# Optimization experiments

Hardware: AMD Instinct MI355X
Metric: run time of the kernel (lower is better)

## Reference

```python
import jax, jax.numpy as jnp
import numpy as np

V, C, E, L, M = 100000, 420000, 1260000, 3, 64
FV = FC = 3
ED = 2


def _gru(x, h, wih, whh, bih, bhh):
    # PyTorch GRUCell semantics. x: [N, in], h: [N, H], wih: [3H, in], whh: [3H, H]
    gi = x @ wih.T + bih
    gh = h @ whh.T + bhh
    H = h.shape[-1]
    r = jax.nn.sigmoid(gi[:, :H] + gh[:, :H])
    z = jax.nn.sigmoid(gi[:, H:2 * H] + gh[:, H:2 * H])
    n = jnp.tanh(gi[:, 2 * H:] + r * gh[:, 2 * H:])
    return (1.0 - z) * n + z * h


def setup_inputs() -> dict:
    key = jax.random.key(0)
    ks = iter(jax.random.split(key, 40))
    f = lambda shape, s=0.1: jax.random.normal(next(ks), shape, jnp.float32) * s
    inp = {
        'var_features': jax.random.normal(next(ks), (V, FV), jnp.float32),
        'clause_features': jax.random.normal(next(ks), (C, FC), jnp.float32),
        'edge_features': jax.random.uniform(next(ks), (E, ED), dtype=jnp.float32),
        'v2c_w1': f((L, M, FV + ED)), 'v2c_b1': f((L, M)),
        'v2c_w2': f((L, M, M)), 'v2c_b2': f((L, M)),
        'c2v_w1': f((L, M, FC + ED)), 'c2v_b1': f((L, M)),
        'c2v_w2': f((L, M, M)), 'c2v_b2': f((L, M)),
        'var_gru_wih': f((L, 3 * FV, M)), 'var_gru_whh': f((L, 3 * FV, FV)),
        'var_gru_bih': f((L, 3 * FV)), 'var_gru_bhh': f((L, 3 * FV)),
        'cls_gru_wih': f((L, 3 * FC, M)), 'cls_gru_whh': f((L, 3 * FC, FC)),
        'cls_gru_bih': f((L, 3 * FC)), 'cls_gru_bhh': f((L, 3 * FC)),
        'att_w1': f((L, M, FC)), 'att_b1': f((L, M)),
        'att_w2': f((L, 1, M)), 'att_b2': f((L, 1)),
        'var_idx': jax.random.randint(next(ks), (E,), 0, V),
        'clause_idx': jax.random.randint(next(ks), (E,), 0, C),
    }
    return inp


def reference(var_features, clause_features, edge_features,
              v2c_w1, v2c_b1, v2c_w2, v2c_b2,
              c2v_w1, c2v_b1, c2v_w2, c2v_b2,
              var_gru_wih, var_gru_whh, var_gru_bih, var_gru_bhh,
              cls_gru_wih, cls_gru_whh, cls_gru_bih, cls_gru_bhh,
              att_w1, att_b1, att_w2, att_b2,
              var_idx, clause_idx):
    vf, cf = var_features, clause_features
    for l in range(L):  # fixed small number of message-passing steps
        # var -> clause: gather, edge MLP, attention-weight, scatter-add
        v2c_in = jnp.concatenate([vf[var_idx], edge_features], axis=1)  # [E, FV+ED]
        m = jnp.maximum(v2c_in @ v2c_w1[l].T + v2c_b1[l], 0.0) @ v2c_w2[l].T + v2c_b2[l]  # [E, M]
        att = (jnp.tanh(cf @ att_w1[l].T + att_b1[l]) @ att_w2[l].T + att_b2[l])[:, 0]  # [C]
        att = jax.nn.softmax(att, axis=0)
        m = m * att[clause_idx][:, None]
        cmsg = jax.ops.segment_sum(m, clause_idx, num_segments=C)  # [C, M]
        cf_new = _gru(cmsg, cf, cls_gru_wih[l], cls_gru_whh[l], cls_gru_bih[l], cls_gru_bhh[l])
        # clause -> var uses OLD clause features (matches torch forward ordering)
        c2v_in = jnp.concatenate([cf[clause_idx], edge_features], axis=1)  # [E, FC+ED]
        mv = jnp.maximum(c2v_in @ c2v_w1[l].T + c2v_b1[l], 0.0) @ c2v_w2[l].T + c2v_b2[l]  # [E, M]
        vmsg = jax.ops.segment_sum(mv, var_idx, num_segments=V)  # [V, M]
        vf = _gru(vmsg, vf, var_gru_wih[l], var_gru_whh[l], var_gru_bih[l], var_gru_bhh[l])
        cf = cf_new
    return jnp.concatenate([vf, cf], axis=0)  # [V+C, 3]
```

## Files before the change

### kernel.cpp

```cpp
#include <hip/hip_runtime.h>
#include <hip/hip_fp16.h>
#include <math.h>

#define V_N 100000
#define C_N 420000
#define E_N 1260000
#define L_N 3

__device__ __forceinline__ float fsig(float x) {
    return 1.0f / (1.0f + __expf(-x));
}
__device__ __forceinline__ float ftanh(float x) {
    x = fminf(fmaxf(x, -15.0f), 15.0f);
    float t = __expf(2.0f * x);
    return (t - 1.0f) / (t + 1.0f);
}

__global__ void k_prep(const float* __restrict__ v2c_w1, const float* __restrict__ v2c_b1,
                       const float* __restrict__ v2c_w2, const float* __restrict__ v2c_b2,
                       const float* __restrict__ c2v_w1, const float* __restrict__ c2v_b1,
                       const float* __restrict__ c2v_w2, const float* __restrict__ c2v_b2,
                       const float* __restrict__ cls_wih, const float* __restrict__ var_wih,
                       float* __restrict__ prep) {
    int t = blockIdx.x * blockDim.x + threadIdx.x;
    if (t >= 6 * 1040) return;
    int s = t / 1040, r = t % 1040;
    int side = s / 3, l = s % 3;
    const float* w1  = (side ? c2v_w1 : v2c_w1) + l * 320;
    const float* b1  = (side ? c2v_b1 : v2c_b1) + l * 64;
    const float* W2  = (side ? c2v_w2 : v2c_w2) + l * 4096;
    const float* b2  = (side ? c2v_b2 : v2c_b2) + l * 64;
    const float* wih = (side ? var_wih : cls_wih) + l * 576;
    float v = 0.0f;
    if (r < 1024) {
        int j = r >> 4, q = r & 15;
        if (q < 5) v = w1[j * 5 + q];
        else if (q == 5) v = b1[j];
        else if (q < 15) {
            int k = q - 6; float a = 0.0f;
            for (int o = 0; o < 64; ++o) a += wih[k * 64 + o] * W2[o * 64 + j];
            v = a;
        }
    } else if (r < 1033) {
        int k = r - 1024; float a = 0.0f;
        for (int o = 0; o < 64; ++o) a += wih[k * 64 + o] * b2[o];
        v = a;
    }
    prep[t] = v;
}

__global__ __launch_bounds__(256) void k_countrank(const int* __restrict__ ci,
                                                   const int* __restrict__ vi,
                                                   int* __restrict__ cntC, int* __restrict__ cntV,
                                                   int* __restrict__ rankC, int* __restrict__ rankV) {
    int e = blockIdx.x * 256 + threadIdx.x;
    if (e >= E_N) return;
    rankC[e] = atomicAdd(&cntC[ci[e]], 1);
    rankV[e] = atomicAdd(&cntV[vi[e]], 1);
}

__global__ __launch_bounds__(256) void k_scanA(const int* __restrict__ cntC,
                                               const int* __restrict__ cntV, int nbC,
                                               int* __restrict__ bsumC, int* __restrict__ bsumV) {
    int b = blockIdx.x, t = threadIdx.x;
    const int* cnt; int N; int* bs; int bb;
    if (b < nbC) { cnt = cntC; N = C_N; bs = bsumC; bb = b; }
    else         { cnt = cntV; N = V_N; bs = bsumV; bb = b - nbC; }
    int base = bb * 1024 + t * 4;
    int s = 0;
    #pragma unroll
    for (int q = 0; q < 4; ++q) { int i = base + q; if (i < N) s += cnt[i]; }
    __shared__ int sh[256];
    sh[t] = s; __syncthreads();
    for (int d = 128; d; d >>= 1) { if (t < d) sh[t] += sh[t + d]; __syncthreads(); }
    if (t == 0) bs[bb] = sh[0];
}

__global__ __launch_bounds__(512) void k_scanB(int* __restrict__ bsumC, int nbC, int* __restrict__ totC,
                                               int* __restrict__ bsumV, int nbV, int* __restrict__ totV) {
    int* bsum = blockIdx.x ? bsumV : bsumC;
    int nb    = blockIdx.x ? nbV : nbC;
    int* tot  = blockIdx.x ? totV : totC;
    __shared__ int sh[512];
    int t = threadIdx.x;
    int v = (t < nb) ? bsum[t] : 0;
    sh[t] = v; __syncthreads();
    for (int d = 1; d < 512; d <<= 1) {
        int add = (t >= d) ? sh[t - d] : 0;
        __syncthreads();
        sh[t] += add;
        __syncthreads();
    }
    if (t < nb) bsum[t] = sh[t] - v;
    if (t == nb - 1) *tot = sh[t];
}

__global__ __launch_bounds__(256) void k_scanC(const int* __restrict__ cntC,
                                               const int* __restrict__ cntV, int nbC,
                                               const int* __restrict__ bsumC,
                                               const int* __restrict__ bsumV,
                                               int* __restrict__ rowC, int* __restrict__ rowV) {
    int b = blockIdx.x, t = threadIdx.x;
    const int* cnt; int N; const int* bs; int* row; int bb;
    if (b < nbC) { cnt = cntC; N = C_N; bs = bsumC; row = rowC; bb = b; }
    else         { cnt = cntV; N = V_N; bs = bsumV; row = rowV; bb = b - nbC; }
    int base = bb * 1024 + t * 4;
    int v[4], local[4];
    #pragma unroll
    for (int q = 0; q < 4; ++q) { int i = base + q; v[q] = (i < N) ? cnt[i] : 0; }
    local[0] = 0; local[1] = v[0]; local[2] = v[0] + v[1]; local[3] = v[0] + v[1] + v[2];
    int mysum = local[3] + v[3];
    __shared__ int sh[256];
    sh[t] = mysum; __syncthreads();
    for (int d = 1; d < 256; d <<= 1) {
        int add = (t >= d) ? sh[t - d] : 0;
        __syncthreads();
        sh[t] += add;
        __syncthreads();
    }
    int excl = sh[t] - mysum + bs[bb];
    #pragma unroll
    for (int q = 0; q < 4; ++q) {
        int i = base + q;
        if (i < N) row[i] = excl + local[q];
    }
}

__global__ __launch_bounds__(256) void k_att(const float* __restrict__ cf,
                                             const float* __restrict__ aw1,
                                             const float* __restrict__ ab1,
                                             const float* __restrict__ aw2,
                                             const float* __restrict__ ab2,
                                             float* __restrict__ logits,
                                             float* __restrict__ pmax,
                                             float* __restrict__ Sg) {
    if (blockIdx.x == 0 && threadIdx.x == 0) Sg[0] = 0.0f;
    int c = blockIdx.x * blockDim.x + threadIdx.x;
    float logit = -1e30f;
    if (c < C_N) {
        float h0 = cf[c * 3], h1 = cf[c * 3 + 1], h2 = cf[c * 3 + 2];
        float acc = ab2[0];
        #pragma unroll
        for (int k = 0; k < 64; ++k) {
            float tv = ftanh(aw1[k * 3] * h0 + aw1[k * 3 + 1] * h1 +
                             aw1[k * 3 + 2] * h2 + ab1[k]);
            acc += aw2[k] * tv;
        }
        logits[c] = acc;
        logit = acc;
    }
    float m = logit;
    #pragma unroll
    for (int off = 32; off; off >>= 1) m = fmaxf(m, __shfl_xor(m, off));
    __shared__ float smax[4];
    int lane = threadIdx.x & 63, wid = threadIdx.x >> 6;
    if (lane == 0) smax[wid] = m;
    __syncthreads();
    if (threadIdx.x == 0)
        pmax[blockIdx.x] = fmaxf(fmaxf(smax[0], smax[1]), fmaxf(smax[2], smax[3]));
}

__global__ __launch_bounds__(256) void k_sum(const float* __restrict__ logits,
                                             const float* __restrict__ pmax, int npmax,
                                             float* __restrict__ Sg) {
    __shared__ float sh[4];
    float m = -1e30f;
    for (int i = threadIdx.x; i < npmax; i += 256) m = fmaxf(m, pmax[i]);
    #pragma unroll
    for (int off = 32; off; off >>= 1) m = fmaxf(m, __shfl_xor(m, off));
    int lane = threadIdx.x & 63, wid = threadIdx.x >> 6;
    if (lane == 0) sh[wid] = m;
    __syncthreads();
    float mm = fmaxf(fmaxf(sh[0], sh[1]), fmaxf(sh[2], sh[3]));
    __syncthreads();
    int c = blockIdx.x * 256 + threadIdx.x;
    float e = (c < C_N) ? __expf(logits[c] - mm) : 0.0f;
    #pragma unroll
    for (int off = 32; off; off >>= 1) e += __shfl_xor(e, off);
    if (lane == 0) sh[wid] = e;
    __syncthreads();
    if (threadIdx.x == 0) {
        unsafeAtomicAdd(&Sg[0], sh[0] + sh[1] + sh[2] + sh[3]);
        if (blockIdx.x == 0) Sg[1] = mm;
    }
}

__global__ __launch_bounds__(256) void k_edge(const float* __restrict__ feat,
                                              const float* __restrict__ ef,
                                              const int* __restrict__ gidx,
                                              const int* __restrict__ didx,
                                              const int* __restrict__ row,
                                              const int* __restrict__ rank,
                                              const float* __restrict__ prep,
                                              uint2* __restrict__ umsg) {
    __shared__ float W[1040];
    for (int i = threadIdx.x; i < 1040; i += 256) W[i] = prep[i];
    __syncthreads();
    int e = blockIdx.x * 256 + threadIdx.x;
    if (e >= E_N) return;
    int g = gidx[e];
    int pos = row[didx[e]] + rank[e];
    float x0 = feat[g * 3], x1 = feat[g * 3 + 1], x2 = feat[g * 3 + 2];
    float2 efv = *(const float2*)(ef + 2 * (size_t)e);
    float u[9];
    #pragma unroll
    for (int k = 0; k < 9; ++k) u[k] = 0.0f;
    for (int j = 0; j < 64; ++j) {
        const float* wj = &W[j * 16];
        float h = wj[0] * x0 + wj[1] * x1 + wj[2] * x2 + wj[3] * efv.x + wj[4] * efv.y + wj[5];
        h = fmaxf(h, 0.0f);
        #pragma unroll
        for (int k = 0; k < 9; ++k) u[k] += wj[6 + k] * h;
    }
    union { __half h[12]; uint2 q[3]; } pk;
    #pragma unroll
    for (int k = 0; k < 9; ++k) pk.h[k] = __float2half(u[k]);
    pk.h[9] = pk.h[10] = pk.h[11] = __float2half(0.0f);
    size_t p = (size_t)pos * 3;
    umsg[p] = pk.q[0]; umsg[p + 1] = pk.q[1]; umsg[p + 2] = pk.q[2];
}

template <bool ATT>
__global__ __launch_bounds__(256) void k_node(const uint2* __restrict__ umsg,
                                              const int* __restrict__ row,
                                              const float* __restrict__ hin,
                                              const float* __restrict__ logits,
                                              const float* __restrict__ Sg,
                                              const float* __restrict__ c2,
                                              const float* __restrict__ whh,
                                              const float* __restrict__ bih,
                                              const float* __restrict__ bhh,
                                              float* __restrict__ hout, int N) {
    int i = blockIdx.x * 256 + threadIdx.x;
    if (i >= N) return;
    int p0 = row[i], p1 = row[i + 1];
    float u[9];
    #pragma unroll
    for (int k = 0; k < 9; ++k) u[k] = 0.0f;
    for (int p = p0; p < p1; ++p) {
        union { __half h[12]; uint2 q[3]; } pk;
        const uint2* r = umsg + (size_t)p * 3;
        pk.q[0] = r[0]; pk.q[1] = r[1]; pk.q[2] = r[2];
        #pragma unroll
        for (int k = 0; k < 9; ++k) u[k] += __half2float(pk.h[k]);
    }
    float cnt = (float)(p1 - p0);
    float scale = 1.0f;
    if (ATT) scale = __expf(logits[i] - Sg[1]) / Sg[0];
    float h0 = hin[i * 3], h1 = hin[i * 3 + 1], h2 = hin[i * 3 + 2];
    float gi[9], gh[9];
    #pragma unroll
    for (int k = 0; k < 9; ++k) gi[k] = scale * (u[k] + cnt * c2[k]) + bih[k];
    #pragma unroll
    for (int k = 0; k < 9; ++k)
        gh[k] = whh[k * 3] * h0 + whh[k * 3 + 1] * h1 + whh[k * 3 + 2] * h2 + bhh[k];
    float r0 = fsig(gi[0] + gh[0]), r1 = fsig(gi[1] + gh[1]), r2 = fsig(gi[2] + gh[2]);
    float z0 = fsig(gi[3] + gh[3]), z1 = fsig(gi[4] + gh[4]), z2 = fsig(gi[5] + gh[5]);
    float n0 = ftanh(gi[6] + r0 * gh[6]);
    float n1 = ftanh(gi[7] + r1 * gh[7]);
    float n2 = ftanh(gi[8] + r2 * gh[8]);
    hout[i * 3 + 0] = (1.0f - z0) * n0 + z0 * h0;
    hout[i * 3 + 1] = (1.0f - z1) * n1 + z1 * h1;
    hout[i * 3 + 2] = (1.0f - z2) * n2 + z2 * h2;
}

extern "C" void kernel_launch(void* const* d_in, const int* in_sizes, int n_in,
                              void* d_out, int out_size, void* d_ws, size_t ws_size,
                              hipStream_t stream) {
    const float* vf0     = (const float*)d_in[0];
    const float* cf0     = (const float*)d_in[1];
    const float* ef      = (const float*)d_in[2];
    const float* v2c_w1  = (const float*)d_in[3];
    const float* v2c_b1  = (const float*)d_in[4];
    const float* v2c_w2  = (const float*)d_in[5];
    const float* v2c_b2  = (const float*)d_in[6];
    const float* c2v_w1  = (const float*)d_in[7];
    const float* c2v_b1  = (const float*)d_in[8];
    const float* c2v_w2  = (const float*)d_in[9];
    const float* c2v_b2  = (const float*)d_in[10];
    const float* var_wih = (const float*)d_in[11];
    const float* var_whh = (const float*)d_in[12];
    const float* var_bih = (const float*)d_in[13];
    const float* var_bhh = (const float*)d_in[14];
    const float* cls_wih = (const float*)d_in[15];
    const float* cls_whh = (const float*)d_in[16];
    const float* cls_bih = (const float*)d_in[17];
    const float* cls_bhh = (const float*)d_in[18];
    const float* att_w1  = (const float*)d_in[19];
    const float* att_b1  = (const float*)d_in[20];
    const float* att_w2  = (const float*)d_in[21];
    const float* att_b2  = (const float*)d_in[22];
    const int*   var_idx = (const int*)d_in[23];
    const int*   cls_idx = (const int*)d_in[24];
    float* dout = (float*)d_out;

    char* w = (char*)d_ws;
    auto alloc = [&](size_t bytes) { char* p = w; w += (bytes + 255) & ~(size_t)255; return p; };
    int*   rowC   = (int*)alloc((C_N + 1) * 4);
    int*   rowV   = (int*)alloc((V_N + 1) * 4);
    int*   cntC   = (int*)alloc((size_t)C_N * 4);
    int*   cntV   = (int*)alloc((size_t)V_N * 4);
    char*  cntEnd = w;
    int*   rankC  = (int*)alloc((size_t)E_N * 4);
    int*   rankV  = (int*)alloc((size_t)E_N * 4);
    int*   bsumC  = (int*)alloc(512 * 4);
    int*   bsumV  = (int*)alloc(512 * 4);
    float* logits = (float*)alloc((size_t)C_N * 4);
    float* pmax   = (float*)alloc(2048 * 4);
    float* Sg     = (float*)alloc(64 * 4);
    float* prep   = (float*)alloc(6 * 1040 * 4);
    uint2* umsg   = (uint2*)alloc((size_t)E_N * 3 * 8);
    float* vfA    = (float*)alloc((size_t)V_N * 3 * 4);
    float* vfB    = (float*)alloc((size_t)V_N * 3 * 4);
    float* cfA    = (float*)alloc((size_t)C_N * 3 * 4);
    float* cfB    = (float*)alloc((size_t)C_N * 3 * 4);

    const int nE  = (E_N + 255) / 256;
    const int nC  = (C_N + 255) / 256;
    const int nV  = (V_N + 255) / 256;
    const int nbC = (C_N + 1023) / 1024;
    const int nbV = (V_N + 1023) / 1024;

    k_prep<<<(6 * 1040 + 255) / 256, 256, 0, stream>>>(
        v2c_w1, v2c_b1, v2c_w2, v2c_b2, c2v_w1, c2v_b1, c2v_w2, c2v_b2,
        cls_wih, var_wih, prep);

    hipMemsetAsync(cntC, 0, (size_t)(cntEnd - (char*)cntC), stream);
    k_countrank<<<nE, 256, 0, stream>>>(cls_idx, var_idx, cntC, cntV, rankC, rankV);
    k_scanA<<<nbC + nbV, 256, 0, stream>>>(cntC, cntV, nbC, bsumC, bsumV);
    k_scanB<<<2, 512, 0, stream>>>(bsumC, nbC, rowC + C_N, bsumV, nbV, rowV + V_N);
    k_scanC<<<nbC + nbV, 256, 0, stream>>>(cntC, cntV, nbC, bsumC, bsumV, rowC, rowV);

    const float* vf_cur = vf0;
    const float* cf_cur = cf0;
    for (int l = 0; l < L_N; ++l) {
        float* vf_next = (l == 0) ? vfA : (l == 1) ? vfB : dout;
        float* cf_next = (l == 0) ? cfA : (l == 1) ? cfB : (dout + (size_t)V_N * 3);

        k_att<<<nC, 256, 0, stream>>>(cf_cur, att_w1 + l * 192, att_b1 + l * 64,
                                      att_w2 + l * 64, att_b2 + l, logits, pmax, Sg);
        k_sum<<<nC, 256, 0, stream>>>(logits, pmax, nC, Sg);

        k_edge<<<nE, 256, 0, stream>>>(vf_cur, ef, var_idx, cls_idx, rowC, rankC,
                                       prep + (0 * 3 + l) * 1040, umsg);
        k_node<true><<<nC, 256, 0, stream>>>(umsg, rowC, cf_cur, logits, Sg,
                                             prep + (0 * 3 + l) * 1040 + 1024,
                                             cls_whh + l * 27, cls_bih + l * 9,
                                             cls_bhh + l * 9, cf_next, C_N);

        k_edge<<<nE, 256, 0, stream>>>(cf_cur, ef, cls_idx, var_idx, rowV, rankV,
                                       prep + (1 * 3 + l) * 1040, umsg);
        k_node<false><<<nV, 256, 0, stream>>>(umsg, rowV, vf_cur, logits, Sg,
                                              prep + (1 * 3 + l) * 1040 + 1024,
                                              var_whh + l * 27, var_bih + l * 9,
                                              var_bhh + l * 9, vf_next, V_N);

        vf_cur = vf_next;
        cf_cur = cf_next;
    }
}
```

Measured before the change: 926.7 us.

## Fuse both edge directions, the softmax sum and next-layer attention into two kernels per layer

```diff
diff --git a/kernel.cpp b/kernel.cpp
--- a/kernel.cpp
+++ b/kernel.cpp
@@ -6,6 +6,9 @@
 #define C_N 420000
 #define E_N 1260000
 #define L_N 3
+#define NCBLK 1641
+#define NVBLK 391
+#define NEBLK 4922
 
 __device__ __forceinline__ float fsig(float x) {
     return 1.0f / (1.0f + __expf(-x));
@@ -126,15 +129,15 @@
     }
 }
 
-__global__ __launch_bounds__(256) void k_att(const float* __restrict__ cf,
-                                             const float* __restrict__ aw1,
-                                             const float* __restrict__ ab1,
-                                             const float* __restrict__ aw2,
-                                             const float* __restrict__ ab2,
-                                             float* __restrict__ logits,
-                                             float* __restrict__ pmax,
-                                             float* __restrict__ Sg) {
-    if (blockIdx.x == 0 && threadIdx.x == 0) Sg[0] = 0.0f;
+__global__ __launch_bounds__(256) void k_att0(const float* __restrict__ cf,
+                                              const float* __restrict__ aw1,
+                                              const float* __restrict__ ab1,
+                                              const float* __restrict__ aw2,
+                                              const float* __restrict__ ab2,
+                                              float* __restrict__ logits,
+                                              float* __restrict__ pmax,
+                                              float* __restrict__ Sg) {
+    if (blockIdx.x == 0 && threadIdx.x < 8) Sg[threadIdx.x] = 0.0f;
     int c = blockIdx.x * blockDim.x + threadIdx.x;
     float logit = -1e30f;
     if (c < C_N) {
@@ -160,108 +163,193 @@
         pmax[blockIdx.x] = fmaxf(fmaxf(smax[0], smax[1]), fmaxf(smax[2], smax[3]));
 }
 
-__global__ __launch_bounds__(256) void k_sum(const float* __restrict__ logits,
-                                             const float* __restrict__ pmax, int npmax,
-                                             float* __restrict__ Sg) {
-    __shared__ float sh[4];
-    float m = -1e30f;
-    for (int i = threadIdx.x; i < npmax; i += 256) m = fmaxf(m, pmax[i]);
-    #pragma unroll
-    for (int off = 32; off; off >>= 1) m = fmaxf(m, __shfl_xor(m, off));
-    int lane = threadIdx.x & 63, wid = threadIdx.x >> 6;
-    if (lane == 0) sh[wid] = m;
-    __syncthreads();
-    float mm = fmaxf(fmaxf(sh[0], sh[1]), fmaxf(sh[2], sh[3]));
-    __syncthreads();
-    int c = blockIdx.x * 256 + threadIdx.x;
-    float e = (c < C_N) ? __expf(logits[c] - mm) : 0.0f;
-    #pragma unroll
-    for (int off = 32; off; off >>= 1) e += __shfl_xor(e, off);
-    if (lane == 0) sh[wid] = e;
-    __syncthreads();
-    if (threadIdx.x == 0) {
-        unsafeAtomicAdd(&Sg[0], sh[0] + sh[1] + sh[2] + sh[3]);
-        if (blockIdx.x == 0) Sg[1] = mm;
-    }
-}
-
-__global__ __launch_bounds__(256) void k_edge(const float* __restrict__ feat,
-                                              const float* __restrict__ ef,
-                                              const int* __restrict__ gidx,
-                                              const int* __restrict__ didx,
-                                              const int* __restrict__ row,
-                                              const int* __restrict__ rank,
-                                              const float* __restrict__ prep,
-                                              uint2* __restrict__ umsg) {
-    __shared__ float W[1040];
-    for (int i = threadIdx.x; i < 1040; i += 256) W[i] = prep[i];
+__global__ __launch_bounds__(256) void k_edgeM(const float* __restrict__ vf,
+                                               const float* __restrict__ cf,
+                                               const float* __restrict__ ef,
+                                               const int* __restrict__ var_idx,
+                                               const int* __restrict__ cls_idx,
+                                               const int* __restrict__ rowC,
+                                               const int* __restrict__ rowV,
+                                               const int* __restrict__ rankC,
+                                               const int* __restrict__ rankV,
+                                               const float* __restrict__ prepA,
+                                               const float* __restrict__ prepB,
+                                               const float* __restrict__ logits,
+                                               const float* __restrict__ pmax,
+                                               float* __restrict__ SgL,
+                                               uint2* __restrict__ umsgC,
+                                               uint2* __restrict__ umsgV) {
+    __shared__ float WA[1040], WB[1040];
+    for (int i = threadIdx.x; i < 1040; i += 256) { WA[i] = prepA[i]; WB[i] = prepB[i]; }
     __syncthreads();
     int e = blockIdx.x * 256 + threadIdx.x;
-    if (e >= E_N) return;
-    int g = gidx[e];
-    int pos = row[didx[e]] + rank[e];
-    float x0 = feat[g * 3], x1 = feat[g * 3 + 1], x2 = feat[g * 3 + 2];
-    float2 efv = *(const float2*)(ef + 2 * (size_t)e);
-    float u[9];
-    #pragma unroll
-    for (int k = 0; k < 9; ++k) u[k] = 0.0f;
-    for (int j = 0; j < 64; ++j) {
-        const float* wj = &W[j * 16];
-        float h = wj[0] * x0 + wj[1] * x1 + wj[2] * x2 + wj[3] * efv.x + wj[4] * efv.y + wj[5];
-        h = fmaxf(h, 0.0f);
-        #pragma unroll
-        for (int k = 0; k < 9; ++k) u[k] += wj[6 + k] * h;
-    }
-    union { __half h[12]; uint2 q[3]; } pk;
-    #pragma unroll
-    for (int k = 0; k < 9; ++k) pk.h[k] = __float2half(u[k]);
-    pk.h[9] = pk.h[10] = pk.h[11] = __float2half(0.0f);
-    size_t p = (size_t)pos * 3;
-    umsg[p] = pk.q[0]; umsg[p + 1] = pk.q[1]; umsg[p + 2] = pk.q[2];
-}
-
-template <bool ATT>
-__global__ __launch_bounds__(256) void k_node(const uint2* __restrict__ umsg,
-                                              const int* __restrict__ row,
-                                              const float* __restrict__ hin,
-                                              const float* __restrict__ logits,
-                                              const float* __restrict__ Sg,
-                                              const float* __restrict__ c2,
-                                              const float* __restrict__ whh,
-                                              const float* __restrict__ bih,
-                                              const float* __restrict__ bhh,
-                                              float* __restrict__ hout, int N) {
-    int i = blockIdx.x * 256 + threadIdx.x;
-    if (i >= N) return;
-    int p0 = row[i], p1 = row[i + 1];
-    float u[9];
-    #pragma unroll
-    for (int k = 0; k < 9; ++k) u[k] = 0.0f;
-    for (int p = p0; p < p1; ++p) {
+    if (e < E_N) {
+        int v = var_idx[e], c = cls_idx[e];
+        float2 efv = *(const float2*)(ef + 2 * (size_t)e);
+        float a0 = vf[v * 3], a1 = vf[v * 3 + 1], a2 = vf[v * 3 + 2];
+        float b0 = cf[c * 3], b1 = cf[c * 3 + 1], b2 = cf[c * 3 + 2];
+        float uC[9], uV[9];
+        #pragma unroll
+        for (int k = 0; k < 9; ++k) { uC[k] = 0.0f; uV[k] = 0.0f; }
+        for (int j = 0; j < 64; ++j) {
+            const float* wj = &WA[j * 16];
+            float h = fmaxf(wj[0] * a0 + wj[1] * a1 + wj[2] * a2 +
+                            wj[3] * efv.x + wj[4] * efv.y + wj[5], 0.0f);
+            const float* qj = &WB[j * 16];
+            float g = fmaxf(qj[0] * b0 + qj[1] * b1 + qj[2] * b2 +
+                            qj[3] * efv.x + qj[4] * efv.y + qj[5], 0.0f);
+            #pragma unroll
+            for (int k = 0; k < 9; ++k) { uC[k] += wj[6 + k] * h; uV[k] += qj[6 + k] * g; }
+        }
         union { __half h[12]; uint2 q[3]; } pk;
-        const uint2* r = umsg + (size_t)p * 3;
-        pk.q[0] = r[0]; pk.q[1] = r[1]; pk.q[2] = r[2];
-        #pragma unroll
-        for (int k = 0; k < 9; ++k) u[k] += __half2float(pk.h[k]);
-    }
-    float cnt = (float)(p1 - p0);
-    float scale = 1.0f;
-    if (ATT) scale = __expf(logits[i] - Sg[1]) / Sg[0];
-    float h0 = hin[i * 3], h1 = hin[i * 3 + 1], h2 = hin[i * 3 + 2];
-    float gi[9], gh[9];
-    #pragma unroll
-    for (int k = 0; k < 9; ++k) gi[k] = scale * (u[k] + cnt * c2[k]) + bih[k];
-    #pragma unroll
-    for (int k = 0; k < 9; ++k)
-        gh[k] = whh[k * 3] * h0 + whh[k * 3 + 1] * h1 + whh[k * 3 + 2] * h2 + bhh[k];
-    float r0 = fsig(gi[0] + gh[0]), r1 = fsig(gi[1] + gh[1]), r2 = fsig(gi[2] + gh[2]);
-    float z0 = fsig(gi[3] + gh[3]), z1 = fsig(gi[4] + gh[4]), z2 = fsig(gi[5] + gh[5]);
-    float n0 = ftanh(gi[6] + r0 * gh[6]);
-    float n1 = ftanh(gi[7] + r1 * gh[7]);
-    float n2 = ftanh(gi[8] + r2 * gh[8]);
-    hout[i * 3 + 0] = (1.0f - z0) * n0 + z0 * h0;
-    hout[i * 3 + 1] = (1.0f - z1) * n1 + z1 * h1;
-    hout[i * 3 + 2] = (1.0f - z2) * n2 + z2 * h2;
+        #pragma unroll
+        for (int k = 0; k < 9; ++k) pk.h[k] = __float2half(uC[k]);
+        pk.h[9] = pk.h[10] = pk.h[11] = __float2half(0.0f);
+        size_t pC = (size_t)(rowC[c] + rankC[e]) * 3;
+        umsgC[pC] = pk.q[0]; umsgC[pC + 1] = pk.q[1]; umsgC[pC + 2] = pk.q[2];
+        #pragma unroll
+        for (int k = 0; k < 9; ++k) pk.h[k] = __float2half(uV[k]);
+        size_t pV = (size_t)(rowV[v] + rankV[e]) * 3;
+        umsgV[pV] = pk.q[0]; umsgV[pV + 1] = pk.q[1]; umsgV[pV + 2] = pk.q[2];
+    }
+    if (blockIdx.x < NCBLK) {
+        __shared__ float sh[4];
+        float m = -1e30f;
+        for (int i = threadIdx.x; i < NCBLK; i += 256) m = fmaxf(m, pmax[i]);
+        #pragma unroll
+        for (int off = 32; off; off >>= 1) m = fmaxf(m, __shfl_xor(m, off));
+        int lane = threadIdx.x & 63, wid = threadIdx.x >> 6;
+        if (lane == 0) sh[wid] = m;
+        __syncthreads();
+        float mm = fmaxf(fmaxf(sh[0], sh[1]), fmaxf(sh[2], sh[3]));
+        __syncthreads();
+        int c = blockIdx.x * 256 + threadIdx.x;
+        float ex = (c < C_N) ? __expf(logits[c] - mm) : 0.0f;
+        #pragma unroll
+        for (int off = 32; off; off >>= 1) ex += __shfl_xor(ex, off);
+        if (lane == 0) sh[wid] = ex;
+        __syncthreads();
+        if (threadIdx.x == 0) {
+            unsafeAtomicAdd(&SgL[0], sh[0] + sh[1] + sh[2] + sh[3]);
+            if (blockIdx.x == 0) SgL[1] = mm;
+        }
+    }
+}
+
+__global__ __launch_bounds__(256) void k_nodeM(const uint2* __restrict__ umsgC,
+                                               const uint2* __restrict__ umsgV,
+                                               const int* __restrict__ rowC,
+                                               const int* __restrict__ rowV,
+                                               const float* __restrict__ cfin,
+                                               const float* __restrict__ vfin,
+                                               float* __restrict__ cfout,
+                                               float* __restrict__ vfout,
+                                               const float* __restrict__ SgL,
+                                               float* __restrict__ logits,
+                                               float* __restrict__ pmax,
+                                               const float* __restrict__ c2C,
+                                               const float* __restrict__ c2V,
+                                               const float* __restrict__ cls_whh,
+                                               const float* __restrict__ cls_bih,
+                                               const float* __restrict__ cls_bhh,
+                                               const float* __restrict__ var_whh,
+                                               const float* __restrict__ var_bih,
+                                               const float* __restrict__ var_bhh,
+                                               const float* __restrict__ aw1,
+                                               const float* __restrict__ ab1,
+                                               const float* __restrict__ aw2,
+                                               const float* __restrict__ ab2,
+                                               int do_att) {
+    int b = blockIdx.x;
+    if (b < NCBLK) {
+        int i = b * 256 + threadIdx.x;
+        float logit = -1e30f;
+        if (i < C_N) {
+            int p0 = rowC[i], p1 = rowC[i + 1];
+            float u[9];
+            #pragma unroll
+            for (int k = 0; k < 9; ++k) u[k] = 0.0f;
+            for (int p = p0; p < p1; ++p) {
+                union { __half h[12]; uint2 q[3]; } pk;
+                const uint2* r = umsgC + (size_t)p * 3;
+                pk.q[0] = r[0]; pk.q[1] = r[1]; pk.q[2] = r[2];
+                #pragma unroll
+                for (int k = 0; k < 9; ++k) u[k] += __half2float(pk.h[k]);
+            }
+            float cnt = (float)(p1 - p0);
+            float scale = __expf(logits[i] - SgL[1]) / SgL[0];
+            float h0 = cfin[i * 3], h1 = cfin[i * 3 + 1], h2 = cfin[i * 3 + 2];
+            float gi[9], gh[9];
+            #pragma unroll
+            for (int k = 0; k < 9; ++k) gi[k] = scale * (u[k] + cnt * c2C[k]) + cls_bih[k];
+            #pragma unroll
+            for (int k = 0; k < 9; ++k)
+                gh[k] = cls_whh[k * 3] * h0 + cls_whh[k * 3 + 1] * h1 + cls_whh[k * 3 + 2] * h2 + cls_bhh[k];
+            float r0 = fsig(gi[0] + gh[0]), r1 = fsig(gi[1] + gh[1]), r2 = fsig(gi[2] + gh[2]);
+            float z0 = fsig(gi[3] + gh[3]), z1 = fsig(gi[4] + gh[4]), z2 = fsig(gi[5] + gh[5]);
+            float n0 = ftanh(gi[6] + r0 * gh[6]);
+            float n1 = ftanh(gi[7] + r1 * gh[7]);
+            float n2 = ftanh(gi[8] + r2 * gh[8]);
+            float o0 = (1.0f - z0) * n0 + z0 * h0;
+            float o1 = (1.0f - z1) * n1 + z1 * h1;
+            float o2 = (1.0f - z2) * n2 + z2 * h2;
+            cfout[i * 3 + 0] = o0;
+            cfout[i * 3 + 1] = o1;
+            cfout[i * 3 + 2] = o2;
+            if (do_att) {
+                float acc = ab2[0];
+                #pragma unroll
+                for (int k = 0; k < 64; ++k) {
+                    float tv = ftanh(aw1[k * 3] * o0 + aw1[k * 3 + 1] * o1 +
+                                     aw1[k * 3 + 2] * o2 + ab1[k]);
+                    acc += aw2[k] * tv;
+                }
+                logits[i] = acc;
+                logit = acc;
+            }
+        }
+        if (do_att) {
+            float m = logit;
+            #pragma unroll
+            for (int off = 32; off; off >>= 1) m = fmaxf(m, __shfl_xor(m, off));
+            __shared__ float smax[4];
+            int lane = threadIdx.x & 63, wid = threadIdx.x >> 6;
+            if (lane == 0) smax[wid] = m;
+            __syncthreads();
+            if (threadIdx.x == 0)
+                pmax[b] = fmaxf(fmaxf(smax[0], smax[1]), fmaxf(smax[2], smax[3]));
+        }
+    } else {
+        int i = (b - NCBLK) * 256 + threadIdx.x;
+        if (i >= V_N) return;
+        int p0 = rowV[i], p1 = rowV[i + 1];
+        float u[9];
+        #pragma unroll
+        for (int k = 0; k < 9; ++k) u[k] = 0.0f;
+        for (int p = p0; p < p1; ++p) {
+            union { __half h[12]; uint2 q[3]; } pk;
+            const uint2* r = umsgV + (size_t)p * 3;
+            pk.q[0] = r[0]; pk.q[1] = r[1]; pk.q[2] = r[2];
+            #pragma unroll
+            for (int k = 0; k < 9; ++k) u[k] += __half2float(pk.h[k]);
+        }
+        float cnt = (float)(p1 - p0);
+        float h0 = vfin[i * 3], h1 = vfin[i * 3 + 1], h2 = vfin[i * 3 + 2];
+        float gi[9], gh[9];
+        #pragma unroll
+        for (int k = 0; k < 9; ++k) gi[k] = u[k] + cnt * c2V[k] + var_bih[k];
+        #pragma unroll
+        for (int k = 0; k < 9; ++k)
+            gh[k] = var_whh[k * 3] * h0 + var_whh[k * 3 + 1] * h1 + var_whh[k * 3 + 2] * h2 + var_bhh[k];
+        float r0 = fsig(gi[0] + gh[0]), r1 = fsig(gi[1] + gh[1]), r2 = fsig(gi[2] + gh[2]);
+        float z0 = fsig(gi[3] + gh[3]), z1 = fsig(gi[4] + gh[4]), z2 = fsig(gi[5] + gh[5]);
+        float n0 = ftanh(gi[6] + r0 * gh[6]);
+        float n1 = ftanh(gi[7] + r1 * gh[7]);
+        float n2 = ftanh(gi[8] + r2 * gh[8]);
+        vfout[i * 3 + 0] = (1.0f - z0) * n0 + z0 * h0;
+        vfout[i * 3 + 1] = (1.0f - z1) * n1 + z1 * h1;
+        vfout[i * 3 + 2] = (1.0f - z2) * n2 + z2 * h2;
+    }
 }
 
 extern "C" void kernel_launch(void* const* d_in, const int* in_sizes, int n_in,
@@ -309,15 +397,11 @@
     float* pmax   = (float*)alloc(2048 * 4);
     float* Sg     = (float*)alloc(64 * 4);
     float* prep   = (float*)alloc(6 * 1040 * 4);
-    uint2* umsg   = (uint2*)alloc((size_t)E_N * 3 * 8);
-    float* vfA    = (float*)alloc((size_t)V_N * 3 * 4);
-    float* vfB    = (float*)alloc((size_t)V_N * 3 * 4);
-    float* cfA    = (float*)alloc((size_t)C_N * 3 * 4);
-    float* cfB    = (float*)alloc((size_t)C_N * 3 * 4);
-
-    const int nE  = (E_N + 255) / 256;
-    const int nC  = (C_N + 255) / 256;
-    const int nV  = (V_N + 255) / 256;
+    uint2* umsgC  = (uint2*)alloc((size_t)E_N * 3 * 8);
+    uint2* umsgV  = (uint2*)alloc((size_t)E_N * 3 * 8);
+    float* vfW    = (float*)alloc((size_t)V_N * 3 * 4);
+    float* cfW    = (float*)alloc((size_t)C_N * 3 * 4);
+
     const int nbC = (C_N + 1023) / 1024;
     const int nbV = (V_N + 1023) / 1024;
 
@@ -326,36 +410,36 @@
         cls_wih, var_wih, prep);
 
     hipMemsetAsync(cntC, 0, (size_t)(cntEnd - (char*)cntC), stream);
-    k_countrank<<<nE, 256, 0, stream>>>(cls_idx, var_idx, cntC, cntV, rankC, rankV);
+    k_countrank<<<NEBLK, 256, 0, stream>>>(cls_idx, var_idx, cntC, cntV, rankC, rankV);
     k_scanA<<<nbC + nbV, 256, 0, stream>>>(cntC, cntV, nbC, bsumC, bsumV);
     k_scanB<<<2, 512, 0, stream>>>(bsumC, nbC, rowC + C_N, bsumV, nbV, rowV + V_N);
     k_scanC<<<nbC + nbV, 256, 0, stream>>>(cntC, cntV, nbC, bsumC, bsumV, rowC, rowV);
 
-    const float* vf_cur = vf0;
-    const float* cf_cur = cf0;
+    k_att0<<<NCBLK, 256, 0, stream>>>(cf0, att_w1, att_b1, att_w2, att_b2,
+                                      logits, pmax, Sg);
+
     for (int l = 0; l < L_N; ++l) {
-        float* vf_next = (l == 0) ? vfA : (l == 1) ? vfB : dout;
-        float* cf_next = (l == 0) ? cfA : (l == 1) ? cfB : (dout + (size_t)V_N * 3);
-
-        k_att<<<nC, 256, 0, stream>>>(cf_cur, att_w1 + l * 192, att_b1 + l * 64,
-                                      att_w2 + l * 64, att_b2 + l, logits, pmax, Sg);
-        k_sum<<<nC, 256, 0, stream>>>(logits, pmax, nC, Sg);
-
-        k_edge<<<nE, 256, 0, stream>>>(vf_cur, ef, var_idx, cls_idx, rowC, rankC,
-                                       prep + (0 * 3 + l) * 1040, umsg);
-        k_node<true><<<nC, 256, 0, stream>>>(umsg, rowC, cf_cur, logits, Sg,
-                                             prep + (0 * 3 + l) * 1040 + 1024,
-                                             cls_whh + l * 27, cls_bih + l * 9,
-                                             cls_bhh + l * 9, cf_next, C_N);
-
-        k_edge<<<nE, 256, 0, stream>>>(cf_cur, ef, cls_idx, var_idx, rowV, rankV,
-                                       prep + (1 * 3 + l) * 1040, umsg);
-        k_node<false><<<nV, 256, 0, stream>>>(umsg, rowV, vf_cur, logits, Sg,
-                                              prep + (1 * 3 + l) * 1040 + 1024,
-                                              var_whh + l * 27, var_bih + l * 9,
-                                              var_bhh + l * 9, vf_next, V_N);
-
-        vf_cur = vf_next;
-        cf_cur = cf_next;
-    }
-}
+        const float* vin = (l == 0) ? vf0 : vfW;
+        const float* cin = (l == 0) ? cf0 : cfW;
+        float* vout = (l == 2) ? dout : vfW;
+        float* cout = (l == 2) ? (dout + (size_t)V_N * 3) : cfW;
+        const float* prepA = prep + l * 1040;
+        const float* prepB = prep + (3 + l) * 1040;
+        int la = (l < 2) ? (l + 1) : 2;
+
+        k_edgeM<<<NEBLK, 256, 0, stream>>>(vin, cin, ef, var_idx, cls_idx,
+                                           rowC, rowV, rankC, rankV,
+                                           prepA, prepB, logits, pmax,
+                                           Sg + 2 * l, umsgC, umsgV);
+
+        k_nodeM<<<NCBLK + NVBLK, 256, 0, stream>>>(umsgC, umsgV, rowC, rowV,
+                                                   cin, vin, cout, vout,
+                                                   Sg + 2 * l, logits, pmax,
+                                                   prepA + 1024, prepB + 1024,
+                                                   cls_whh + l * 27, cls_bih + l * 9, cls_bhh + l * 9,
+                                                   var_whh + l * 27, var_bih + l * 9, var_bhh + l * 9,
+                                                   att_w1 + la * 192, att_b1 + la * 64,
+                                                   att_w2 + la * 64, att_b2 + la,
+                                                   (l < 2) ? 1 : 0);
+    }
+}
```

After: 806.3 us. 13.0% less time.
